# Performance work log

Hardware: AMD Instinct MI355X
Metric: run time of the kernel (lower is better)

Reference implementation:

```python
import jax, jax.numpy as jnp
import numpy as np

D_EMB, D_HID, D_LAT, K = 512, 512, 256, 7
SEQ, BATCH = 512, 128


def setup_inputs() -> dict:
    key = jax.random.key(0)
    ks = jax.random.split(key, 10)
    x = jax.random.normal(ks[0], (SEQ, BATCH, D_EMB), jnp.float32)
    z = jax.random.normal(ks[1], (SEQ // 4, BATCH, D_LAT), jnp.float32)
    # Conv1d(d_latent, 2*d_hidden, K, groups=d_latent): weight [2*dh, 1, K]
    conv0_w = jax.random.normal(ks[2], (2 * D_HID, 1, K), jnp.float32) * 0.2
    conv0_b = jax.random.normal(ks[3], (2 * D_HID,), jnp.float32) * 0.1
    # Conv1d(d_hidden, 2*d_hidden, K, groups=d_hidden): weight [2*dh, 1, K]
    conv1_w = jax.random.normal(ks[4], (2 * D_HID, 1, K), jnp.float32) * 0.2
    conv1_b = jax.random.normal(ks[5], (2 * D_HID,), jnp.float32) * 0.1
    # LSTM(input=d_emb+d_hid, hidden=d_emb): gate order i,f,g,o
    gin = D_EMB + D_HID
    w_ih = jax.random.normal(ks[6], (4 * D_EMB, gin), jnp.float32) * (1.0 / np.sqrt(gin))
    w_hh = jax.random.normal(ks[7], (4 * D_EMB, D_EMB), jnp.float32) * (1.0 / np.sqrt(D_EMB))
    b_ih = jax.random.normal(ks[8], (4 * D_EMB,), jnp.float32) * 0.05
    b_hh = jax.random.normal(ks[9], (4 * D_EMB,), jnp.float32) * 0.05
    return {"x": x, "z": z, "conv0_w": conv0_w, "conv0_b": conv0_b,
            "conv1_w": conv1_w, "conv1_b": conv1_b,
            "w_ih": w_ih, "w_hh": w_hh, "b_ih": b_ih, "b_hh": b_hh}


def _upsample(z, w, b):
    # z: [L, B, Cin] -> depthwise-grouped conv + relu -> reshape doubles length
    zb = jnp.transpose(z, (1, 2, 0))  # [B, Cin, L]
    groups = zb.shape[1]              # groups = in_channels (weight I-dim is 1)
    pad = w.shape[-1] // 2
    y = jax.lax.conv_general_dilated(
        zb, w, window_strides=(1,), padding=[(pad, pad)],
        dimension_numbers=("NCH", "OIH", "NCH"), feature_group_count=groups)
    y = jax.nn.relu(y + b[None, :, None])          # [B, 2*dh, L]
    B, C2, L = y.shape
    y = jnp.transpose(y, (0, 2, 1)).reshape(B, 2 * L, C2 // 2)
    return jnp.transpose(y, (1, 0, 2))             # [2L, B, dh]


def reference(x, z, conv0_w, conv0_b, conv1_w, conv1_b, w_ih, w_hh, b_ih, b_hh):
    # eval mode: input/word dropout and weight dropout are identity
    z = _upsample(z, conv0_w, conv0_b)
    z = _upsample(z, conv1_w, conv1_b)   # [SEQ, B, d_hidden]
    inp = jnp.concatenate([x[:-1], z[1:]], axis=-1)  # [SEQ-1, B, d_emb+d_hid]
    # precompute input-to-gate projection across all timesteps
    gates_x = jnp.einsum("tbi,gi->tbg", inp, w_ih) + b_ih + b_hh
    H = w_hh.shape[1]
    B = inp.shape[1]

    def step(carry, gx):
        h, c = carry
        gates = gx + h @ w_hh.T
        i, f, g, o = jnp.split(gates, 4, axis=-1)
        c = jax.nn.sigmoid(f) * c + jax.nn.sigmoid(i) * jnp.tanh(g)
        h = jax.nn.sigmoid(o) * jnp.tanh(c)
        return (h, c), h

    h0 = jnp.zeros((B, H), inp.dtype)
    _, hs = jax.lax.scan(step, (h0, h0), gates_x)
    return hs  # [SEQ-1, B, d_embedding]
```

## Files before the change

### kernel.cpp

```cpp
#include <hip/hip_runtime.h>
#include <hip/hip_bf16.h>

typedef unsigned short u16;
typedef unsigned long long u64;
typedef short bf16x8 __attribute__((ext_vector_type(8)));
typedef float f32x4 __attribute__((ext_vector_type(4)));

__device__ __forceinline__ float ldbf(const u16* p) {
    __hip_bfloat16 h = *(const __hip_bfloat16*)p;
    return __bfloat162float(h);
}
__device__ __forceinline__ void stbf(u16* p, float f) {
    *(__hip_bfloat16*)p = __float2bfloat16(f);
}
__device__ __forceinline__ u16 f2bfu(float f) {
    __hip_bfloat16 h = __float2bfloat16(f);
    return *(u16*)&h;
}
__device__ __forceinline__ float bf2f(u16 v) {
    union { unsigned u; float f; } x; x.u = ((unsigned)v) << 16; return x.f;
}
__device__ __forceinline__ float sigm(float x) {
    return 1.0f / (1.0f + __expf(-x));
}

__global__ __launch_bounds__(256) void cvt_bf16(const float* __restrict__ in,
                                                u16* __restrict__ out, int n) {
    int i = blockIdx.x * 256 + threadIdx.x;
    if (i < n) stbf(out + i, in[i]);
}

template <bool INF32>
__global__ __launch_bounds__(256) void upsample(const void* __restrict__ in_,
                                                const float* __restrict__ w,
                                                const float* __restrict__ bias_,
                                                u16* __restrict__ out,
                                                int Lin, int shift) {
    const int Cin = 1024 >> shift;
    const int total = 2 * Lin * 128 * 512;
    int idx = blockIdx.x * 256 + threadIdx.x;
    if (idx >= total) return;
    const int c  = idx & 511;
    const int bb = (idx >> 9) & 127;
    const int tp = idx >> 16;
    const int s  = tp & 1;
    const int l  = tp >> 1;
    const int oc = c + (s << 9);
    const int ch = oc >> shift;
    float acc = bias_[oc];
    #pragma unroll
    for (int k = 0; k < 7; ++k) {
        int li = l + k - 3;
        if (li >= 0 && li < Lin) {
            size_t off = ((size_t)li * 128 + bb) * Cin + ch;
            float v = INF32 ? ((const float*)in_)[off] : ldbf((const u16*)in_ + off);
            acc += w[oc * 7 + k] * v;
        }
    }
    stbf(out + idx, fmaxf(acc, 0.0f));
}

__global__ __launch_bounds__(256) void gemm_gates(const float* __restrict__ x,
                                                  const u16* __restrict__ z2,
                                                  const float* __restrict__ wih,
                                                  const float* __restrict__ bih,
                                                  const float* __restrict__ bhh,
                                                  u16* __restrict__ gates) {
    __shared__ __align__(16) u16 smA[128 * 32];
    __shared__ __align__(16) u16 smB[128 * 32];
    const int tid  = threadIdx.x;
    const int lane = tid & 63;
    const int wave = tid >> 6;
    const int wm = wave >> 1, wn = wave & 1;
    const size_t mbase = (size_t)blockIdx.x * 128;
    const size_t nbase = (size_t)blockIdx.y * 128;

    f32x4 acc[4][4] = {};

    const int srow = tid >> 1;
    const int scol = (tid & 1) * 16;

    for (int kt = 0; kt < 32; ++kt) {
        const int kb = kt * 32;
        if (kb < 512) {
            const float* src = x + (mbase + srow) * 512 + kb + scol;
            alignas(16) u16 tmp[16];
            #pragma unroll
            for (int q = 0; q < 16; ++q) stbf(&tmp[q], src[q]);
            *(int4*)&smA[srow * 32 + scol]     = *(const int4*)&tmp[0];
            *(int4*)&smA[srow * 32 + scol + 8] = *(const int4*)&tmp[8];
        } else {
            const u16* src = z2 + 65536 + (mbase + srow) * 512 + (kb - 512) + scol;
            *(int4*)&smA[srow * 32 + scol]     = *(const int4*)(src);
            *(int4*)&smA[srow * 32 + scol + 8] = *(const int4*)(src + 8);
        }
        {
            const float* src = wih + (nbase + srow) * 1024 + kb + scol;
            alignas(16) u16 tmp[16];
            #pragma unroll
            for (int q = 0; q < 16; ++q) stbf(&tmp[q], src[q]);
            *(int4*)&smB[srow * 32 + scol]     = *(const int4*)&tmp[0];
            *(int4*)&smB[srow * 32 + scol + 8] = *(const int4*)&tmp[8];
        }
        __syncthreads();

        bf16x8 af[4], bfr[4];
        #pragma unroll
        for (int mi = 0; mi < 4; ++mi)
            af[mi] = *(const bf16x8*)&smA[(wm * 64 + mi * 16 + (lane & 15)) * 32 + (lane >> 4) * 8];
        #pragma unroll
        for (int ni = 0; ni < 4; ++ni)
            bfr[ni] = *(const bf16x8*)&smB[(wn * 64 + ni * 16 + (lane & 15)) * 32 + (lane >> 4) * 8];
        #pragma unroll
        for (int mi = 0; mi < 4; ++mi)
            #pragma unroll
            for (int ni = 0; ni < 4; ++ni)
                acc[mi][ni] = __builtin_amdgcn_mfma_f32_16x16x32_bf16(af[mi], bfr[ni], acc[mi][ni], 0, 0, 0);
        __syncthreads();
    }

    u16* gt = gates + (size_t)blockIdx.x * 262144;
    #pragma unroll
    for (int ni = 0; ni < 4; ++ni) {
        const int n = (int)nbase + wn * 64 + ni * 16 + (lane & 15);
        const float bias = bih[n] + bhh[n];
        const int g  = n >> 9;
        const int jh = n & 511;
        u16* gb = gt + (size_t)(jh >> 4) * 8192 + (size_t)(g * 16 + (jh & 15));
        #pragma unroll
        for (int mi = 0; mi < 4; ++mi) {
            const int b = wm * 64 + mi * 16 + (lane >> 4) * 4;
            #pragma unroll
            for (int r = 0; r < 4; ++r)
                stbf(gb + (size_t)(b + r) * 64, acc[mi][ni][r] + bias);
        }
    }
}

__global__ __launch_bounds__(256) void lstm_persist(const u16* __restrict__ gates,
                                                    const u16* __restrict__ whh,
                                                    u16* __restrict__ hbuf,
                                                    float* __restrict__ out,
                                                    unsigned* __restrict__ bar) {
    __shared__ __align__(16) u16 smW[32768];
    __shared__ __align__(16) u16 smH[16384];
    __shared__ __align__(16) float smG[4 * 32 * 18];

    const int tid  = threadIdx.x;
    const int lane = tid & 63;
    const int wave = tid >> 6;
    const int bid  = blockIdx.x;
    const int grp  = bid >> 5;
    const int jt   = bid & 31;
    const int b0   = grp << 5;
    const int jh0  = jt << 4;
    unsigned* gbar = bar + grp * 64;

    for (int i = tid; i < 4096; i += 256) {
        const int row = i >> 6;
        const int c8  = i & 63;
        const u16* src = whh + ((size_t)((row >> 4) * 512 + jh0 + (row & 15))) * 512 + c8 * 8;
        int4 v = *(const int4*)src;
        int byte = row * 1024 + c8 * 16;
        byte ^= (row & 7) << 4;
        *(int4*)((char*)smW + byte) = v;
    }

    const int fr = lane & 15;
    const int kq = lane >> 4;
    const int br = tid >> 3;
    const int j2 = (tid & 7) * 2;
    float cA = 0.0f, cB = 0.0f;

    __syncthreads();

    for (int t = 0; t < 511; ++t) {
        const u64* hp = (const u64*)(hbuf + (size_t)(t & 1) * 65536 + (size_t)b0 * 512);
        u64 tmp[16];
        #pragma unroll
        for (int i = 0; i < 16; ++i)
            tmp[i] = __hip_atomic_load(hp + i * 256 + tid,
                                       __ATOMIC_RELAXED, __HIP_MEMORY_SCOPE_AGENT);
        __builtin_amdgcn_sched_barrier(0);
        #pragma unroll
        for (int i = 0; i < 16; ++i) {
            const int e   = i * 256 + tid;
            const int row = e >> 7;
            const int c4  = e & 127;
            const int byte = (row * 1024 + c4 * 8) ^ ((row & 7) << 4);
            *(u64*)((char*)smH + byte) = tmp[i];
        }
        const u16* gsrc = gates + (size_t)t * 262144 + (size_t)jt * 8192 + (size_t)b0 * 64;
        unsigned gx4[4];
        #pragma unroll
        for (int g = 0; g < 4; ++g)
            gx4[g] = *(const unsigned*)(gsrc + br * 64 + g * 16 + j2);

        __syncthreads();

        f32x4 acc0 = {}, acc1 = {};
        const int brow = wave * 16 + fr;
        const int bxor = (brow & 7) << 4;
        const int axor = (fr & 7) << 4;
        #pragma unroll
        for (int kt = 0; kt < 16; ++kt) {
            const int kb = kt * 64 + kq * 16;
            bf16x8 bf = *(const bf16x8*)((const char*)smW + ((brow * 1024 + kb) ^ bxor));
            bf16x8 a0 = *(const bf16x8*)((const char*)smH + ((fr * 1024 + kb) ^ axor));
            bf16x8 a1 = *(const bf16x8*)((const char*)smH + (((16 + fr) * 1024 + kb) ^ axor));
            acc0 = __builtin_amdgcn_mfma_f32_16x16x32_bf16(a0, bf, acc0, 0, 0, 0);
            acc1 = __builtin_amdgcn_mfma_f32_16x16x32_bf16(a1, bf, acc1, 0, 0, 0);
        }

        #pragma unroll
        for (int r = 0; r < 4; ++r) {
            smG[(wave * 32 + kq * 4 + r) * 18 + fr]      = acc0[r];
            smG[(wave * 32 + 16 + kq * 4 + r) * 18 + fr] = acc1[r];
        }
        __syncthreads();

        u16*   hdst = hbuf + (size_t)((t + 1) & 1) * 65536;
        float* odst = out + ((size_t)t * 128 + b0 + br) * 512 + jh0;
        float hn0, hn1;
        {
            const float gi = smG[(0 * 32 + br) * 18 + j2] + bf2f((u16)(gx4[0] & 0xffff));
            const float gf = smG[(1 * 32 + br) * 18 + j2] + bf2f((u16)(gx4[1] & 0xffff));
            const float gg = smG[(2 * 32 + br) * 18 + j2] + bf2f((u16)(gx4[2] & 0xffff));
            const float go = smG[(3 * 32 + br) * 18 + j2] + bf2f((u16)(gx4[3] & 0xffff));
            cA = sigm(gf) * cA + sigm(gi) * tanhf(gg);
            hn0 = sigm(go) * tanhf(cA);
        }
        {
            const float gi = smG[(0 * 32 + br) * 18 + j2 + 1] + bf2f((u16)(gx4[0] >> 16));
            const float gf = smG[(1 * 32 + br) * 18 + j2 + 1] + bf2f((u16)(gx4[1] >> 16));
            const float gg = smG[(2 * 32 + br) * 18 + j2 + 1] + bf2f((u16)(gx4[2] >> 16));
            const float go = smG[(3 * 32 + br) * 18 + j2 + 1] + bf2f((u16)(gx4[3] >> 16));
            cB = sigm(gf) * cB + sigm(gi) * tanhf(gg);
            hn1 = sigm(go) * tanhf(cB);
        }
        {
            const unsigned hw = (unsigned)f2bfu(hn0) | ((unsigned)f2bfu(hn1) << 16);
            __hip_atomic_store((unsigned*)(hdst + (size_t)(b0 + br) * 512 + jh0 + j2),
                               hw, __ATOMIC_RELAXED, __HIP_MEMORY_SCOPE_AGENT);
        }
        *(float2*)(odst + j2) = make_float2(hn0, hn1);

        if (t < 510) {
            asm volatile("s_waitcnt vmcnt(0)" ::: "memory");
            __syncthreads();
            if (tid == 0) {
                __hip_atomic_fetch_add(gbar, 1u,
                                       __ATOMIC_RELAXED, __HIP_MEMORY_SCOPE_AGENT);
                const unsigned tgt = (unsigned)(t + 1) * 32u;
                while (__hip_atomic_load(gbar, __ATOMIC_RELAXED,
                                         __HIP_MEMORY_SCOPE_AGENT) < tgt)
                    __builtin_amdgcn_s_sleep(2);
            }
            __syncthreads();
            asm volatile("" ::: "memory");
        }
    }
}

extern "C" void kernel_launch(void* const* d_in, const int* in_sizes, int n_in,
                              void* d_out, int out_size, void* d_ws, size_t ws_size,
                              hipStream_t stream) {
    const float* x   = (const float*)d_in[0];
    const float* z   = (const float*)d_in[1];
    const float* c0w = (const float*)d_in[2];
    const float* c0b = (const float*)d_in[3];
    const float* c1w = (const float*)d_in[4];
    const float* c1b = (const float*)d_in[5];
    const float* wih = (const float*)d_in[6];
    const float* whh = (const float*)d_in[7];
    const float* bih = (const float*)d_in[8];
    const float* bhh = (const float*)d_in[9];
    float* out = (float*)d_out;
    char* ws = (char*)d_ws;

    u16*      z1     = (u16*)(ws);
    u16*      z2     = (u16*)(ws + 33554432);
    u16*      gates  = (u16*)(ws + 100663296);
    unsigned* bar    = (unsigned*)(ws + 368574464);
    u16*      hbuf   = (u16*)(ws + 368836608);
    u16*      whh_bf = (u16*)(ws + 369098752);

    hipMemsetAsync(bar, 0, 1024, stream);
    hipMemsetAsync(hbuf, 0, 131072, stream);

    cvt_bf16<<<dim3(4096), 256, 0, stream>>>(whh, whh_bf, 1048576);

    upsample<true ><<<dim3(16777216 / 256), 256, 0, stream>>>(z,  c0w, c0b, z1, 128, 2);
    upsample<false><<<dim3(33554432 / 256), 256, 0, stream>>>(z1, c1w, c1b, z2, 256, 1);

    gemm_gates<<<dim3(511, 16), 256, 0, stream>>>(x, z2, wih, bih, bhh, gates);

    {
        const u16* gates_a = gates;
        const u16* whh_a   = whh_bf;
        u16*       hbuf_a  = hbuf;
        float*     out_a   = out;
        unsigned*  bar_a   = bar;
        void* args[] = {&gates_a, &whh_a, &hbuf_a, &out_a, &bar_a};
        hipLaunchCooperativeKernel((void*)lstm_persist, dim3(128), dim3(256),
                                   args, 0, stream);
    }
}
```

Measured before the change: 3.349 ms.

## Use per-block flags for group barrier, keep W_hh fragments in registers, fast tanh

The shared atomic counter barrier in the persistent LSTM kernel is replaced by per-block step flags. Each block publishes its own flag, and one wave polls all 32 peer flags in parallel with no sleep, which removes contention on a single atomic and cuts the wakeup latency. The recurrent weight fragments are hoisted out of the time loop into registers, removing the per-step LDS reads of W_hh at the cost of extra VGPR pressure. tanhf is replaced by an exp-based approximation, which may lose some accuracy or overflow for large inputs.

Result: faster. 3.123 ms (-6.7%).

```diff
diff --git a/kernel.cpp b/kernel.cpp
--- a/kernel.cpp
+++ b/kernel.cpp
@@ -22,6 +22,10 @@
 }
 __device__ __forceinline__ float sigm(float x) {
     return 1.0f / (1.0f + __expf(-x));
+}
+__device__ __forceinline__ float tanh_fast(float x) {
+    float e = __expf(2.0f * x);
+    return 1.0f - 2.0f / (e + 1.0f);
 }
 
 __global__ __launch_bounds__(256) void cvt_bf16(const float* __restrict__ in,
@@ -141,7 +145,7 @@
                                                     const u16* __restrict__ whh,
                                                     u16* __restrict__ hbuf,
                                                     float* __restrict__ out,
-                                                    unsigned* __restrict__ bar) {
+                                                    unsigned* __restrict__ flags) {
     __shared__ __align__(16) u16 smW[32768];
     __shared__ __align__(16) u16 smH[16384];
     __shared__ __align__(16) float smG[4 * 32 * 18];
@@ -154,7 +158,7 @@
     const int jt   = bid & 31;
     const int b0   = grp << 5;
     const int jh0  = jt << 4;
-    unsigned* gbar = bar + grp * 64;
+    unsigned* myflag = flags + grp * 2048 + jt * 64;
 
     for (int i = tid; i < 4096; i += 256) {
         const int row = i >> 6;
@@ -174,6 +178,14 @@
 
     __syncthreads();
 
+    const int brow = wave * 16 + fr;
+    const int bxor = (brow & 7) << 4;
+    const int axor = (fr & 7) << 4;
+    bf16x8 wfrag[16];
+    #pragma unroll
+    for (int kt = 0; kt < 16; ++kt)
+        wfrag[kt] = *(const bf16x8*)((const char*)smW + ((brow * 1024 + kt * 64 + kq * 16) ^ bxor));
+
     for (int t = 0; t < 511; ++t) {
         const u64* hp = (const u64*)(hbuf + (size_t)(t & 1) * 65536 + (size_t)b0 * 512);
         u64 tmp[16];
@@ -199,17 +211,13 @@
         __syncthreads();
 
         f32x4 acc0 = {}, acc1 = {};
-        const int brow = wave * 16 + fr;
-        const int bxor = (brow & 7) << 4;
-        const int axor = (fr & 7) << 4;
         #pragma unroll
         for (int kt = 0; kt < 16; ++kt) {
             const int kb = kt * 64 + kq * 16;
-            bf16x8 bf = *(const bf16x8*)((const char*)smW + ((brow * 1024 + kb) ^ bxor));
             bf16x8 a0 = *(const bf16x8*)((const char*)smH + ((fr * 1024 + kb) ^ axor));
             bf16x8 a1 = *(const bf16x8*)((const char*)smH + (((16 + fr) * 1024 + kb) ^ axor));
-            acc0 = __builtin_amdgcn_mfma_f32_16x16x32_bf16(a0, bf, acc0, 0, 0, 0);
-            acc1 = __builtin_amdgcn_mfma_f32_16x16x32_bf16(a1, bf, acc1, 0, 0, 0);
+            acc0 = __builtin_amdgcn_mfma_f32_16x16x32_bf16(a0, wfrag[kt], acc0, 0, 0, 0);
+            acc1 = __builtin_amdgcn_mfma_f32_16x16x32_bf16(a1, wfrag[kt], acc1, 0, 0, 0);
         }
 
         #pragma unroll
@@ -227,16 +235,16 @@
             const float gf = smG[(1 * 32 + br) * 18 + j2] + bf2f((u16)(gx4[1] & 0xffff));
             const float gg = smG[(2 * 32 + br) * 18 + j2] + bf2f((u16)(gx4[2] & 0xffff));
             const float go = smG[(3 * 32 + br) * 18 + j2] + bf2f((u16)(gx4[3] & 0xffff));
-            cA = sigm(gf) * cA + sigm(gi) * tanhf(gg);
-            hn0 = sigm(go) * tanhf(cA);
+            cA = sigm(gf) * cA + sigm(gi) * tanh_fast(gg);
+            hn0 = sigm(go) * tanh_fast(cA);
         }
         {
             const float gi = smG[(0 * 32 + br) * 18 + j2 + 1] + bf2f((u16)(gx4[0] >> 16));
             const float gf = smG[(1 * 32 + br) * 18 + j2 + 1] + bf2f((u16)(gx4[1] >> 16));
             const float gg = smG[(2 * 32 + br) * 18 + j2 + 1] + bf2f((u16)(gx4[2] >> 16));
             const float go = smG[(3 * 32 + br) * 18 + j2 + 1] + bf2f((u16)(gx4[3] >> 16));
-            cB = sigm(gf) * cB + sigm(gi) * tanhf(gg);
-            hn1 = sigm(go) * tanhf(cB);
+            cB = sigm(gf) * cB + sigm(gi) * tanh_fast(gg);
+            hn1 = sigm(go) * tanh_fast(cB);
         }
         {
             const unsigned hw = (unsigned)f2bfu(hn0) | ((unsigned)f2bfu(hn1) << 16);
@@ -248,13 +256,18 @@
         if (t < 510) {
             asm volatile("s_waitcnt vmcnt(0)" ::: "memory");
             __syncthreads();
-            if (tid == 0) {
-                __hip_atomic_fetch_add(gbar, 1u,
-                                       __ATOMIC_RELAXED, __HIP_MEMORY_SCOPE_AGENT);
-                const unsigned tgt = (unsigned)(t + 1) * 32u;
-                while (__hip_atomic_load(gbar, __ATOMIC_RELAXED,
-                                         __HIP_MEMORY_SCOPE_AGENT) < tgt)
-                    __builtin_amdgcn_s_sleep(2);
+            if (tid == 0)
+                __hip_atomic_store(myflag, (unsigned)(t + 1),
+                                   __ATOMIC_RELAXED, __HIP_MEMORY_SCOPE_AGENT);
+            if (wave == 0) {
+                const unsigned tgt = (unsigned)(t + 1);
+                unsigned* fp = flags + grp * 2048 + lane * 64;
+                int done = (lane >= 32 || lane == jt) ? 1 : 0;
+                while (!__all(done)) {
+                    if (!done)
+                        done = (__hip_atomic_load(fp, __ATOMIC_RELAXED,
+                                                  __HIP_MEMORY_SCOPE_AGENT) >= tgt);
+                }
             }
             __syncthreads();
             asm volatile("" ::: "memory");
@@ -281,11 +294,11 @@
     u16*      z1     = (u16*)(ws);
     u16*      z2     = (u16*)(ws + 33554432);
     u16*      gates  = (u16*)(ws + 100663296);
-    unsigned* bar    = (unsigned*)(ws + 368574464);
+    unsigned* flags  = (unsigned*)(ws + 368574464);
     u16*      hbuf   = (u16*)(ws + 368836608);
     u16*      whh_bf = (u16*)(ws + 369098752);
 
-    hipMemsetAsync(bar, 0, 1024, stream);
+    hipMemsetAsync(flags, 0, 32768, stream);
     hipMemsetAsync(hbuf, 0, 131072, stream);
 
     cvt_bf16<<<dim3(4096), 256, 0, stream>>>(whh, whh_bf, 1048576);
@@ -300,8 +313,8 @@
         const u16* whh_a   = whh_bf;
         u16*       hbuf_a  = hbuf;
         float*     out_a   = out;
-        unsigned*  bar_a   = bar;
-        void* args[] = {&gates_a, &whh_a, &hbuf_a, &out_a, &bar_a};
+        unsigned*  flags_a = flags;
+        void* args[] = {&gates_a, &whh_a, &hbuf_a, &out_a, &flags_a};
         hipLaunchCooperativeKernel((void*)lstm_persist, dim3(128), dim3(256),
                                    args, 0, stream);
     }
```
